# Kernel tuning notes

Hardware: AMD Instinct MI355X
Metric: run time of the kernel (lower is better)

Reference implementation:

```python
import jax, jax.numpy as jnp
import numpy as np

NEG_SLOPE = 0.2


def setup_inputs() -> dict:
    key = jax.random.key(0)
    kx, ka, kW, kav = jax.random.split(key, 4)
    B, V, H, D = 8, 2048, 256, 128
    x = jax.random.normal(kx, (B, V, H), dtype=jnp.float32)
    adjacency_matrix = jax.random.randint(ka, (V, V), 0, 2, dtype=jnp.int32)
    W = jax.random.normal(kW, (D, H), dtype=jnp.float32) * 0.05  # Linear(H->D), weight [out,in]
    a = jax.random.normal(kav, (1, 2 * D), dtype=jnp.float32) * 0.05  # Linear(2D->1)
    return {"x": x, "adjacency_matrix": adjacency_matrix, "W": W, "a": a}


def reference(x, adjacency_matrix, W, a):
    B, V, H = x.shape
    D = W.shape[0]
    # p = W(x): [B,V,D]
    p = jnp.einsum('bvh,dh->bvd', x, W)
    # a(cat(p_i, p_j)) == a_left.p_i + a_right.p_j ; leaky_relu applied to the sum (same math,
    # avoids materializing the O(B*V^2*2D) repeat/concat tensor)
    a_left, a_right = a[0, :D], a[0, D:]
    e_i = p @ a_left    # [B,V]
    e_j = p @ a_right   # [B,V]
    scores = jax.nn.leaky_relu(e_i[:, :, None] + e_j[:, None, :], negative_slope=NEG_SLOPE)  # [B,V,V]
    weights = jax.nn.softmax(scores, axis=-1)
    adj = adjacency_matrix.astype(weights.dtype)[None]  # [1,V,V]
    weights_masked = weights * adj
    # renormalize masked weights to the (unmasked) row mass
    weights_masked = weights_masked * (
        jnp.sum(weights, axis=-1, keepdims=True) / jnp.sum(weights_masked, axis=-1, keepdims=True)
    )
    # weighted sum over neighbors j: sum_j w[b,i,j] * p[b,j,:]
    attentioned = jnp.einsum('bij,bjd->bid', weights_masked, p)
    return jax.nn.relu(attentioned)
```

## Files before the change

kernel.cpp:

```cpp
#include <hip/hip_runtime.h>
#include <hip/hip_bf16.h>

#define BATCH 8
#define V 2048
#define H 256
#define D 128

typedef __attribute__((ext_vector_type(8))) _Float16 f16x8;
typedef __attribute__((ext_vector_type(4))) float f32x4;
typedef unsigned int uint32;

static __device__ __forceinline__ uint32 pk2(float lo, float hi) {
  __fp16 __attribute__((ext_vector_type(2))) h = __builtin_amdgcn_cvt_pkrtz(lo, hi);
  uint32 u;
  __builtin_memcpy(&u, &h, 4);
  return u;
}

__global__ __launch_bounds__(256) void k_pack(const int* __restrict__ adj,
                                              const float* __restrict__ W,
                                              unsigned int* __restrict__ pk,
                                              float* __restrict__ Wt) {
  const int blk = blockIdx.x;
  if (blk < V) {
    const int w = threadIdx.x >> 6, lane = threadIdx.x & 63;
    const int* row = adj + (size_t)blk * V;
#pragma unroll
    for (int it = 0; it < 8; ++it) {
      const int j = it * 256 + w * 64 + lane;
      unsigned long long m = __ballot(row[j] != 0);
      if (lane < 2)
        pk[blk * 64 + it * 8 + w * 2 + lane] = (unsigned int)(m >> (lane * 32));
    }
  } else {
    const int d = blk - V;
    Wt[(size_t)threadIdx.x * D + d] = W[(size_t)d * H + threadIdx.x];
  }
}

__global__ __launch_bounds__(256, 2) void k_proj(const float* __restrict__ x,
                                                 const float* __restrict__ Wt,
                                                 const float* __restrict__ a,
                                                 _Float16* __restrict__ pTf,
                                                 float* __restrict__ ei,
                                                 _Float16* __restrict__ Fh,
                                                 _Float16* __restrict__ Ph) {
  __shared__ float xs[32 * H];
  __shared__ _Float16 st[128][52];
  const int t = threadIdx.x;
  const int b = blockIdx.x >> 6;
  const int j0 = (blockIdx.x & 63) * 32;
  {
    const float4* xsrc = (const float4*)(x + ((size_t)b * V + j0) * H);
    float4* xdst = (float4*)xs;
#pragma unroll
    for (int q = 0; q < 8; ++q) xdst[t + 256 * q] = xsrc[t + 256 * q];
  }
  __syncthreads();

  const int dq = t & 31;
  const int jg = t >> 5;
  float acc[4][4];
#pragma unroll
  for (int k = 0; k < 4; ++k)
#pragma unroll
    for (int dd = 0; dd < 4; ++dd) acc[k][dd] = 0.f;

  const float* wbase = Wt + dq * 4;
  const float* xbase = xs + jg * 4 * H;
#pragma unroll 2
  for (int h4 = 0; h4 < 64; ++h4) {
    float4 wv[4], xv[4];
#pragma unroll
    for (int hh = 0; hh < 4; ++hh)
      wv[hh] = *(const float4*)(wbase + (size_t)(h4 * 4 + hh) * D);
#pragma unroll
    for (int k = 0; k < 4; ++k)
      xv[k] = *(const float4*)(xbase + k * H + h4 * 4);
#pragma unroll
    for (int k = 0; k < 4; ++k)
#pragma unroll
      for (int dd = 0; dd < 4; ++dd)
        acc[k][dd] += xv[k].x * ((const float*)&wv[0])[dd] +
                      xv[k].y * ((const float*)&wv[1])[dd] +
                      xv[k].z * ((const float*)&wv[2])[dd] +
                      xv[k].w * ((const float*)&wv[3])[dd];
  }

  const float4 aLv = *(const float4*)(a + dq * 4);
  const float4 aRv = *(const float4*)(a + D + dq * 4);
#pragma unroll
  for (int k = 0; k < 4; ++k) {
    float te = acc[k][0] * aLv.x + acc[k][1] * aLv.y + acc[k][2] * aLv.z + acc[k][3] * aLv.w;
    float tf = acc[k][0] * aRv.x + acc[k][1] * aRv.y + acc[k][2] * aRv.z + acc[k][3] * aRv.w;
#pragma unroll
    for (int off = 1; off < 32; off <<= 1) {
      te += __shfl_xor(te, off, 64);
      tf += __shfl_xor(tf, off, 64);
    }
    if (dq == 0) {
      const size_t row = (size_t)b * V + j0 + jg * 4 + k;
      ei[row] = te;
      Fh[row] = (_Float16)__expf(tf);
      Ph[row] = (_Float16)__expf(0.2f * tf);
    }
  }

#pragma unroll
  for (int dd = 0; dd < 4; ++dd) {
    union { uint32 u[2]; unsigned long long ll; } pk_;
    pk_.u[0] = pk2(acc[0][dd], acc[1][dd]);
    pk_.u[1] = pk2(acc[2][dd], acc[3][dd]);
    *(unsigned long long*)&st[dq * 4 + dd][jg * 4] = pk_.ll;
  }
  __syncthreads();

  const int c = (blockIdx.x & 63) >> 1;
  const int ks = blockIdx.x & 1;
  const int lane = t & 63, g = t >> 6;
#pragma unroll
  for (int ff = 0; ff < 2; ++ff) {
    const int dt = ff * 4 + g;
    const int dR = dt * 16 + (lane & 15);
    const int jc = (lane >> 4) * 8;
    union { unsigned long long ll[2]; f16x8 v; } vv_;
    vv_.ll[0] = *(const unsigned long long*)&st[dR][jc];
    vv_.ll[1] = *(const unsigned long long*)&st[dR][jc + 4];
    *(f16x8*)((char*)pTf +
              (((((size_t)b * 32 + c) * 8 + dt) * 2 + ks) * 64 + lane) * 16) = vv_.v;
  }
}


typedef union { uint4 v; uint32 u[4]; } U4;
typedef union { uint32 u[4]; f16x8 v; } AFu;
struct PFS {
  U4 FH0, FH1, PH0, PH1, M0, M1;
  AFu AF0, AF1;
  uint32 w0, w1;
};

#define PKMUL(d, a, b) asm("v_pk_mul_f16 %0, %1, %2" : "=v"(d) : "v"(a), "v"(b));
#define PKMAX(d, a, b) asm("v_pk_max_f16 %0, %1, %2" : "=v"(d) : "v"(a), "v"(b));

#define WGEN1(AF, FH_, PH_, MSK_)                        \
  {                                                      \
    _Pragma("unroll") for (int p_ = 0; p_ < 4; ++p_) {   \
      uint32 t0_, t1_;                                   \
      PKMUL(t0_, Ei2, (FH_).u[p_])                       \
      PKMUL(t1_, Eip2, (PH_).u[p_])                      \
      PKMAX(t0_, t0_, t1_)                               \
      (AF).u[p_] = t0_ & (MSK_).u[p_];                   \
    }                                                    \
  }

#define WGEN(S)                      \
  WGEN1(S.AF0, S.FH0, S.PH0, S.M0)   \
  WGEN1(S.AF1, S.FH1, S.PH1, S.M1)

#define LUTREAD(S)                          \
  S.M0.v = lut[(S.w0 >> kq8) & 0xFF];       \
  S.M1.v = lut[(S.w1 >> kq8) & 0xFF];

#define PFETCH(S, C)                                      \
  {                                                       \
    const char* f_ = fbase + (C) * 128 + kq16;            \
    const char* p_ = pbase + (C) * 128 + kq16;            \
    S.FH0.v = *(const uint4*)(f_);                        \
    S.FH1.v = *(const uint4*)(f_ + 64);                   \
    S.PH0.v = *(const uint4*)(p_);                        \
    S.PH1.v = *(const uint4*)(p_ + 64);                   \
    S.w0 = adjp[iRb + (C) * 2];                           \
    S.w1 = adjp[iRb + (C) * 2 + 1];                       \
  }

#define LOADB(BR, C)                                      \
  {                                                       \
    const char* g_ = gbase + (size_t)(C) * 16384;         \
    _Pragma("unroll") for (int q_ = 0; q_ < 8; ++q_)      \
      BR[q_] = *(const f16x8*)(g_ + q_ * 1024);           \
  }

#define DOMFMA(S, BX)                                                                  \
  _Pragma("unroll") for (int nt_ = 0; nt_ < 4; ++nt_) {                                \
    acc0[nt_] = __builtin_amdgcn_mfma_f32_16x16x32_f16(S.AF0.v, BX[2 * nt_], acc0[nt_], 0, 0, 0);     \
    acc1[nt_] = __builtin_amdgcn_mfma_f32_16x16x32_f16(S.AF1.v, BX[2 * nt_ + 1], acc1[nt_], 0, 0, 0); \
  }                                                                                    \
  accS0 = __builtin_amdgcn_mfma_f32_16x16x32_f16(S.AF0.v, onesv, accS0, 0, 0, 0);      \
  accS1 = __builtin_amdgcn_mfma_f32_16x16x32_f16(S.AF1.v, onesv, accS1, 0, 0, 0);

#define BODYF(C, SX, BX, SY)  \
  {                           \
    DOMFMA(SX, BX)            \
    LUTREAD(SY)               \
    WGEN(SY)                  \
    LOADB(BX, (C) + 2)        \
    PFETCH(SX, (C) + 2)       \
  }

__global__ __launch_bounds__(256, 2) void k_attn(
    const _Float16* __restrict__ pTf,
    const float* __restrict__ ei,
    const _Float16* __restrict__ Fht,
    const _Float16* __restrict__ Pht,
    const unsigned int* __restrict__ adjp,
    float* __restrict__ out) {
  __shared__ uint4 lut[256];
  {
    const int tb = threadIdx.x;
    const uint32 m0 = ((tb & 1) ? 0xFFFFu : 0u) | ((tb & 2) ? 0xFFFF0000u : 0u);
    const uint32 m1 = ((tb & 4) ? 0xFFFFu : 0u) | ((tb & 8) ? 0xFFFF0000u : 0u);
    const uint32 m2 = ((tb & 16) ? 0xFFFFu : 0u) | ((tb & 32) ? 0xFFFF0000u : 0u);
    const uint32 m3 = ((tb & 64) ? 0xFFFFu : 0u) | ((tb & 128) ? 0xFFFF0000u : 0u);
    lut[tb] = make_uint4(m0, m1, m2, m3);
  }
  __syncthreads();

  const int t = threadIdx.x, lane = t & 63, wave = t >> 6;
  const int pay = (blockIdx.x & 7) * 64 + (blockIdx.x >> 3);
  const int bdh = pay >> 5;
  const int ig = pay & 31;
  const int b = bdh >> 1, dh = bdh & 1;
  const int i0 = ig * 64 + wave * 16;
  const int kq = lane >> 4;
  const int kq8 = kq * 8;
  const int kq16 = kq * 16;
  const int iR = i0 + (lane & 15);
  const int iRb = iR * 64;
  const float eiv = ei[(size_t)b * V + iR];
  const float Eif = __expf(eiv);
  const float Eipf = __expf(0.2f * eiv);
  const uint32 Ei2 = pk2(Eif, Eif);
  const uint32 Eip2 = pk2(Eipf, Eipf);
  const char* fbase = (const char*)(Fht + (size_t)b * V);
  const char* pbase = (const char*)(Pht + (size_t)b * V);
  const size_t fb0 = ((size_t)b * 32) * 16384 + (size_t)dh * 8192;
  const char* gbase = (const char*)pTf + fb0 + lane * 16;

  union { uint32 u[4]; f16x8 v; } ones_;
  ones_.u[0] = ones_.u[1] = ones_.u[2] = ones_.u[3] = 0x3C003C00u;
  const f16x8 onesv = ones_.v;

  f32x4 acc0[4], acc1[4];
#pragma unroll
  for (int nt = 0; nt < 4; ++nt) {
    acc0[nt] = (f32x4){0.f, 0.f, 0.f, 0.f};
    acc1[nt] = (f32x4){0.f, 0.f, 0.f, 0.f};
  }
  f32x4 accS0 = (f32x4){0.f, 0.f, 0.f, 0.f};
  f32x4 accS1 = (f32x4){0.f, 0.f, 0.f, 0.f};

  f16x8 bA[8], bB[8];
  PFS sA, sB;

  LOADB(bA, 0)
  LOADB(bB, 1)
  PFETCH(sA, 0)
  PFETCH(sB, 1)
  LUTREAD(sA)
  WGEN(sA)

  for (int c2 = 0; c2 < 15; ++c2) {
    const int c = c2 * 2;
    BODYF(c, sA, bA, sB)
    BODYF(c + 1, sB, bB, sA)
  }
  {
    DOMFMA(sA, bA)
    LUTREAD(sB)
    WGEN(sB)
  }
  { DOMFMA(sB, bB) }

  float* ob = out + ((size_t)b * V + i0) * D + dh * 64 + (lane & 15);
#pragma unroll
  for (int r = 0; r < 4; ++r) {
    const float inv_ = 1.0f / (accS0[r] + accS1[r]);
#pragma unroll
    for (int nt = 0; nt < 4; ++nt) {
      const float v = (acc0[nt][r] + acc1[nt][r]) * inv_;
      ob[(size_t)(kq * 4 + r) * D + nt * 16] = fmaxf(v, 0.f);
    }
  }
}

extern "C" void kernel_launch(void* const* d_in, const int* in_sizes, int n_in,
                              void* d_out, int out_size, void* d_ws, size_t ws_size,
                              hipStream_t stream) {
  const float* x = (const float*)d_in[0];
  const int* adj = (const int*)d_in[1];
  const float* W = (const float*)d_in[2];
  const float* a = (const float*)d_in[3];
  float* out = (float*)d_out;

  char* ws = (char*)d_ws;
  _Float16* pTf = (_Float16*)ws;
  float* ei = (float*)(ws + (4u << 20));
  _Float16* Fh = (_Float16*)(ws + (4u << 20) + 65536);
  _Float16* Ph = (_Float16*)(ws + (4u << 20) + 98304);
  unsigned int* adjp = (unsigned int*)(ws + (4u << 20) + 131072);
  float* Wt = (float*)(ws + (4u << 20) + 131072 + 524288);

  k_pack<<<dim3(V + D), dim3(256), 0, stream>>>(adj, W, adjp, Wt);
  k_proj<<<dim3(BATCH * (V / 32)), dim3(256), 0, stream>>>(x, Wt, a, pTf, ei, Fh, Ph);
  k_attn<<<dim3(BATCH * 2 * (V / 64)), dim3(256), 0, stream>>>(pTf, ei, Fh, Ph, adjp, out);
}
```

Measured before the change: 58.51 us.

## Use f16 MFMA for projection and precompute W^T a vectors for scores

Replaces the scalar FP32 FMA projection in k_proj with 16x16x32 f16 MFMA instructions that read x and W directly from global memory, dropping the LDS staging of x and the W transpose. The attention logit vectors are now computed as x·(W^T a_left) and x·(W^T a_right), with those two vectors precomputed in one extra k_pack block. The logits stay in fp32 from the raw x, while the projection is rounded to f16 inputs. Loads are no longer staged through shared memory, and each block re-reads W from global or L2.

```diff
diff --git a/kernel.cpp b/kernel.cpp
--- a/kernel.cpp
+++ b/kernel.cpp
@@ -19,8 +19,10 @@
 
 __global__ __launch_bounds__(256) void k_pack(const int* __restrict__ adj,
                                               const float* __restrict__ W,
+                                              const float* __restrict__ a,
                                               unsigned int* __restrict__ pk,
-                                              float* __restrict__ Wt) {
+                                              float* __restrict__ vL,
+                                              float* __restrict__ vR) {
   const int blk = blockIdx.x;
   if (blk < V) {
     const int w = threadIdx.x >> 6, lane = threadIdx.x & 63;
@@ -33,96 +35,114 @@
         pk[blk * 64 + it * 8 + w * 2 + lane] = (unsigned int)(m >> (lane * 32));
     }
   } else {
-    const int d = blk - V;
-    Wt[(size_t)threadIdx.x * D + d] = W[(size_t)d * H + threadIdx.x];
-  }
-}
+    const int h = threadIdx.x;
+    float sL = 0.f, sR = 0.f;
+    for (int d = 0; d < D; ++d) {
+      const float wv = W[(size_t)d * H + h];
+      sL += wv * a[d];
+      sR += wv * a[D + d];
+    }
+    vL[h] = sL;
+    vR[h] = sR;
+  }
+}
+
+#define DOT4(s, xv, vv) \
+  s += (xv).x * (vv).x + (xv).y * (vv).y + (xv).z * (vv).z + (xv).w * (vv).w;
 
 __global__ __launch_bounds__(256, 2) void k_proj(const float* __restrict__ x,
-                                                 const float* __restrict__ Wt,
-                                                 const float* __restrict__ a,
+                                                 const float* __restrict__ W,
+                                                 const float* __restrict__ vL,
+                                                 const float* __restrict__ vR,
                                                  _Float16* __restrict__ pTf,
                                                  float* __restrict__ ei,
                                                  _Float16* __restrict__ Fh,
                                                  _Float16* __restrict__ Ph) {
-  __shared__ float xs[32 * H];
   __shared__ _Float16 st[128][52];
-  const int t = threadIdx.x;
+  const int t = threadIdx.x, lane = t & 63, wave = t >> 6;
   const int b = blockIdx.x >> 6;
   const int j0 = (blockIdx.x & 63) * 32;
-  {
-    const float4* xsrc = (const float4*)(x + ((size_t)b * V + j0) * H);
-    float4* xdst = (float4*)xs;
-#pragma unroll
-    for (int q = 0; q < 8; ++q) xdst[t + 256 * q] = xsrc[t + 256 * q];
-  }
-  __syncthreads();
-
-  const int dq = t & 31;
-  const int jg = t >> 5;
-  float acc[4][4];
-#pragma unroll
-  for (int k = 0; k < 4; ++k)
-#pragma unroll
-    for (int dd = 0; dd < 4; ++dd) acc[k][dd] = 0.f;
-
-  const float* wbase = Wt + dq * 4;
-  const float* xbase = xs + jg * 4 * H;
-#pragma unroll 2
-  for (int h4 = 0; h4 < 64; ++h4) {
-    float4 wv[4], xv[4];
-#pragma unroll
-    for (int hh = 0; hh < 4; ++hh)
-      wv[hh] = *(const float4*)(wbase + (size_t)(h4 * 4 + hh) * D);
-#pragma unroll
-    for (int k = 0; k < 4; ++k)
-      xv[k] = *(const float4*)(xbase + k * H + h4 * 4);
-#pragma unroll
-    for (int k = 0; k < 4; ++k)
-#pragma unroll
-      for (int dd = 0; dd < 4; ++dd)
-        acc[k][dd] += xv[k].x * ((const float*)&wv[0])[dd] +
-                      xv[k].y * ((const float*)&wv[1])[dd] +
-                      xv[k].z * ((const float*)&wv[2])[dd] +
-                      xv[k].w * ((const float*)&wv[3])[dd];
-  }
-
-  const float4 aLv = *(const float4*)(a + dq * 4);
-  const float4 aRv = *(const float4*)(a + D + dq * 4);
-#pragma unroll
-  for (int k = 0; k < 4; ++k) {
-    float te = acc[k][0] * aLv.x + acc[k][1] * aLv.y + acc[k][2] * aLv.z + acc[k][3] * aLv.w;
-    float tf = acc[k][0] * aRv.x + acc[k][1] * aRv.y + acc[k][2] * aRv.z + acc[k][3] * aRv.w;
-#pragma unroll
-    for (int off = 1; off < 32; off <<= 1) {
-      te += __shfl_xor(te, off, 64);
-      tf += __shfl_xor(tf, off, 64);
-    }
-    if (dq == 0) {
-      const size_t row = (size_t)b * V + j0 + jg * 4 + k;
-      ei[row] = te;
-      Fh[row] = (_Float16)__expf(tf);
-      Ph[row] = (_Float16)__expf(0.2f * tf);
-    }
-  }
-
-#pragma unroll
-  for (int dd = 0; dd < 4; ++dd) {
-    union { uint32 u[2]; unsigned long long ll; } pk_;
-    pk_.u[0] = pk2(acc[0][dd], acc[1][dd]);
-    pk_.u[1] = pk2(acc[2][dd], acc[3][dd]);
-    *(unsigned long long*)&st[dq * 4 + dd][jg * 4] = pk_.ll;
-  }
+  const int kq = lane >> 4, l15 = lane & 15;
+
+  const float* wrow0 = W + (size_t)(wave * 32 + l15) * H + kq * 8;
+  const float* wrow1 = wrow0 + 16 * H;
+  const float* xrow0 = x + ((size_t)(b * V + j0 + l15)) * H + kq * 8;
+  const float* xrow1 = xrow0 + 16 * H;
+  const float* vLp = vL + kq * 8;
+  const float* vRp = vR + kq * 8;
+
+  f32x4 acc[2][2];
+#pragma unroll
+  for (int i_ = 0; i_ < 2; ++i_)
+#pragma unroll
+    for (int j_ = 0; j_ < 2; ++j_) acc[i_][j_] = (f32x4){0.f, 0.f, 0.f, 0.f};
+  float eL0 = 0.f, eL1 = 0.f, eR0 = 0.f, eR1 = 0.f;
+
+  typedef union { uint32 u[4]; f16x8 v; } AFu;
+#pragma unroll
+  for (int ks = 0; ks < 8; ++ks) {
+    const int ho = ks * 32;
+    const float4 w0a = *(const float4*)(wrow0 + ho), w0b = *(const float4*)(wrow0 + ho + 4);
+    const float4 w1a = *(const float4*)(wrow1 + ho), w1b = *(const float4*)(wrow1 + ho + 4);
+    const float4 x0a = *(const float4*)(xrow0 + ho), x0b = *(const float4*)(xrow0 + ho + 4);
+    const float4 x1a = *(const float4*)(xrow1 + ho), x1b = *(const float4*)(xrow1 + ho + 4);
+    AFu aw0, aw1, bx0, bx1;
+    aw0.u[0] = pk2(w0a.x, w0a.y); aw0.u[1] = pk2(w0a.z, w0a.w);
+    aw0.u[2] = pk2(w0b.x, w0b.y); aw0.u[3] = pk2(w0b.z, w0b.w);
+    aw1.u[0] = pk2(w1a.x, w1a.y); aw1.u[1] = pk2(w1a.z, w1a.w);
+    aw1.u[2] = pk2(w1b.x, w1b.y); aw1.u[3] = pk2(w1b.z, w1b.w);
+    bx0.u[0] = pk2(x0a.x, x0a.y); bx0.u[1] = pk2(x0a.z, x0a.w);
+    bx0.u[2] = pk2(x0b.x, x0b.y); bx0.u[3] = pk2(x0b.z, x0b.w);
+    bx1.u[0] = pk2(x1a.x, x1a.y); bx1.u[1] = pk2(x1a.z, x1a.w);
+    bx1.u[2] = pk2(x1b.x, x1b.y); bx1.u[3] = pk2(x1b.z, x1b.w);
+    acc[0][0] = __builtin_amdgcn_mfma_f32_16x16x32_f16(aw0.v, bx0.v, acc[0][0], 0, 0, 0);
+    acc[0][1] = __builtin_amdgcn_mfma_f32_16x16x32_f16(aw0.v, bx1.v, acc[0][1], 0, 0, 0);
+    acc[1][0] = __builtin_amdgcn_mfma_f32_16x16x32_f16(aw1.v, bx0.v, acc[1][0], 0, 0, 0);
+    acc[1][1] = __builtin_amdgcn_mfma_f32_16x16x32_f16(aw1.v, bx1.v, acc[1][1], 0, 0, 0);
+    if (wave == 0) {
+      const float4 vla = *(const float4*)(vLp + ho), vlb = *(const float4*)(vLp + ho + 4);
+      const float4 vra = *(const float4*)(vRp + ho), vrb = *(const float4*)(vRp + ho + 4);
+      DOT4(eL0, x0a, vla) DOT4(eL0, x0b, vlb)
+      DOT4(eL1, x1a, vla) DOT4(eL1, x1b, vlb)
+      DOT4(eR0, x0a, vra) DOT4(eR0, x0b, vrb)
+      DOT4(eR1, x1a, vra) DOT4(eR1, x1b, vrb)
+    }
+  }
+
+  if (wave == 0) {
+    eL0 += __shfl_xor(eL0, 16, 64); eL0 += __shfl_xor(eL0, 32, 64);
+    eL1 += __shfl_xor(eL1, 16, 64); eL1 += __shfl_xor(eL1, 32, 64);
+    eR0 += __shfl_xor(eR0, 16, 64); eR0 += __shfl_xor(eR0, 32, 64);
+    eR1 += __shfl_xor(eR1, 16, 64); eR1 += __shfl_xor(eR1, 32, 64);
+    if (lane < 16) {
+      const size_t r0 = (size_t)b * V + j0 + lane;
+      ei[r0] = eL0;
+      Fh[r0] = (_Float16)__expf(eR0);
+      Ph[r0] = (_Float16)__expf(0.2f * eR0);
+      const size_t r1 = r0 + 16;
+      ei[r1] = eL1;
+      Fh[r1] = (_Float16)__expf(eR1);
+      Ph[r1] = (_Float16)__expf(0.2f * eR1);
+    }
+  }
+
+#pragma unroll
+  for (int t_ = 0; t_ < 2; ++t_)
+#pragma unroll
+    for (int jt = 0; jt < 2; ++jt)
+#pragma unroll
+      for (int r = 0; r < 4; ++r)
+        st[(wave * 2 + t_) * 16 + kq * 4 + r][jt * 16 + l15] = (_Float16)acc[t_][jt][r];
   __syncthreads();
 
   const int c = (blockIdx.x & 63) >> 1;
   const int ks = blockIdx.x & 1;
-  const int lane = t & 63, g = t >> 6;
+  const int g = t >> 6;
 #pragma unroll
   for (int ff = 0; ff < 2; ++ff) {
     const int dt = ff * 4 + g;
-    const int dR = dt * 16 + (lane & 15);
-    const int jc = (lane >> 4) * 8;
+    const int dR = dt * 16 + l15;
+    const int jc = kq * 8;
     union { unsigned long long ll[2]; f16x8 v; } vv_;
     vv_.ll[0] = *(const unsigned long long*)&st[dR][jc];
     vv_.ll[1] = *(const unsigned long long*)&st[dR][jc + 4];
@@ -299,9 +319,10 @@
   _Float16* Fh = (_Float16*)(ws + (4u << 20) + 65536);
   _Float16* Ph = (_Float16*)(ws + (4u << 20) + 98304);
   unsigned int* adjp = (unsigned int*)(ws + (4u << 20) + 131072);
-  float* Wt = (float*)(ws + (4u << 20) + 131072 + 524288);
-
-  k_pack<<<dim3(V + D), dim3(256), 0, stream>>>(adj, W, adjp, Wt);
-  k_proj<<<dim3(BATCH * (V / 32)), dim3(256), 0, stream>>>(x, Wt, a, pTf, ei, Fh, Ph);
+  float* vL = (float*)(ws + (4u << 20) + 131072 + 524288);
+  float* vR = (float*)(ws + (4u << 20) + 131072 + 524288 + 1024);
+
+  k_pack<<<dim3(V + 1), dim3(256), 0, stream>>>(adj, W, a, adjp, vL, vR);
+  k_proj<<<dim3(BATCH * (V / 32)), dim3(256), 0, stream>>>(x, W, vL, vR, pTf, ei, Fh, Ph);
   k_attn<<<dim3(BATCH * 2 * (V / 64)), dim3(256), 0, stream>>>(pTf, ei, Fh, Ph, adjp, out);
 }
```

Result: no change. 58.90 us (+0.7%).
